# Performance work log

Hardware: AMD Instinct MI355X
Metric: run time of the kernel (lower is better)

The kernel has to match this reference:

```python
import jax, jax.numpy as jnp
import numpy as np

N, E = 50000, 800000
D, H, C, ED = 128, 8, 16, 4  # embed_dim, heads, head_dim, edge_dim


def _add_self_loops(edge_index, ea, n):
    # PyG add_self_loops with fill_value='mean': self-loop edge_attr is the
    # mean of incoming edge attributes per destination node (0 if none).
    src, dst = edge_index[0], edge_index[1]
    deg = jax.ops.segment_sum(jnp.ones((src.shape[0],), ea.dtype), dst, num_segments=n)
    loop_ea = jax.ops.segment_sum(ea, dst, num_segments=n) / jnp.maximum(deg, 1.0)[:, None]
    ar = jnp.arange(n, dtype=src.dtype)
    return (jnp.concatenate([src, ar]), jnp.concatenate([dst, ar]),
            jnp.concatenate([ea, loop_ea], axis=0))


def _gatv2(x, src, dst, ea, Wl, bl, Wr, br, We, att, bias, concat):
    n = x.shape[0]
    xl = (x @ Wl + bl).reshape(n, H, C)   # lin_l -> messages (source)
    xr = (x @ Wr + br).reshape(n, H, C)   # lin_r -> target
    e = (ea @ We).reshape(-1, H, C)       # lin_edge (no bias in PyG)
    m = jax.nn.leaky_relu(xl[src] + xr[dst] + e, negative_slope=0.2)  # [Etot,H,C]
    alpha = jnp.einsum('ehc,hc->eh', m, att)
    amax = jax.ops.segment_max(alpha, dst, num_segments=n)   # every node has a self loop
    ex = jnp.exp(alpha - amax[dst])
    den = jax.ops.segment_sum(ex, dst, num_segments=n)
    a = ex / den[dst]                                        # segment softmax over dst
    out = jax.ops.segment_sum(xl[src] * a[:, :, None], dst, num_segments=n)  # [N,H,C]
    out = out.reshape(n, H * C) if concat else out.mean(axis=1)
    return out + bias


def _ln(h, g, b):
    mu = h.mean(-1, keepdims=True)
    var = jnp.var(h, axis=-1, keepdims=True)
    return (h - mu) / jnp.sqrt(var + 1e-5) * g + b


def setup_inputs() -> dict:
    key = jax.random.key(0)
    ks = jax.random.split(key, 32)
    s = 0.05
    inp = {
        'x': jax.random.normal(ks[0], (N, D), jnp.float32),
        'edge_index': jax.random.randint(ks[1], (2, E), 0, N, jnp.int32),
        'edge_attr': jax.random.normal(ks[2], (E, ED), jnp.float32),
    }
    dims = [(D, H * C), (H * C, H * C), (H * C, C)]  # (in_dim, bias_dim per layer)
    k = 3
    for i, (din, bdim) in enumerate(dims):
        inp[f'Wl{i}'] = jax.random.normal(ks[k], (din, H * C), jnp.float32) * s; k += 1
        inp[f'bl{i}'] = jnp.zeros((H * C,), jnp.float32)
        inp[f'Wr{i}'] = jax.random.normal(ks[k], (din, H * C), jnp.float32) * s; k += 1
        inp[f'br{i}'] = jnp.zeros((H * C,), jnp.float32)
        inp[f'We{i}'] = jax.random.normal(ks[k], (ED, H * C), jnp.float32) * s; k += 1
        inp[f'att{i}'] = jax.random.normal(ks[k], (H, C), jnp.float32) * s; k += 1
        inp[f'b{i}'] = jnp.zeros((bdim,), jnp.float32)
        inp[f'g{i}'] = jnp.ones((bdim,), jnp.float32)
        inp[f'be{i}'] = jnp.zeros((bdim,), jnp.float32)
    inp['Wout'] = jax.random.normal(ks[k], (C, D), jnp.float32) * s
    inp['bout'] = jnp.zeros((D,), jnp.float32)
    return inp


def reference(x, edge_index, edge_attr,
              Wl0, bl0, Wr0, br0, We0, att0, b0, g0, be0,
              Wl1, bl1, Wr1, br1, We1, att1, b1, g1, be1,
              Wl2, bl2, Wr2, br2, We2, att2, b2, g2, be2,
              Wout, bout):
    n = x.shape[0]
    src, dst, ea = _add_self_loops(edge_index, edge_attr, n)
    layers = [
        (Wl0, bl0, Wr0, br0, We0, att0, b0, g0, be0, True),
        (Wl1, bl1, Wr1, br1, We1, att1, b1, g1, be1, True),
        (Wl2, bl2, Wr2, br2, We2, att2, b2, g2, be2, False),
    ]
    for (Wl, bl, Wr, br, We, att, bias, g, be, concat) in layers:
        h = _gatv2(x, src, dst, ea, Wl, bl, Wr, br, We, att, bias, concat)
        h = jax.nn.elu(h)
        h = _ln(h, g, be)
        if h.shape == x.shape:  # residual (layers 0,1)
            h = h + x
        x = h
    return x @ Wout + bout
```

## Files before the change

kernel.cpp:

```cpp
#include <hip/hip_runtime.h>
#include <hip/hip_bf16.h>

#define ND 128
#define NH 8
#define NC 16

static inline size_t alignup(size_t x){ return (x + 255) & ~size_t(255); }

__device__ __forceinline__ ushort f2bf(float f){
    __hip_bfloat16 h = __float2bfloat16(f);
    return *reinterpret_cast<ushort*>(&h);
}

__device__ __forceinline__ float hred8(float x){
    int y;
    y = __builtin_amdgcn_mov_dpp(__float_as_int(x), 0xB1, 0xF, 0xF, true);
    x += __int_as_float(y);
    y = __builtin_amdgcn_mov_dpp(__float_as_int(x), 0x4E, 0xF, 0xF, true);
    x += __int_as_float(y);
    y = __builtin_amdgcn_mov_dpp(__float_as_int(x), 0x141, 0xF, 0xF, true);
    x += __int_as_float(y);
    return x;
}


__global__ void hist_kernel(const int* __restrict__ dsts, int* __restrict__ deg, int E)
{
    int e = blockIdx.x * blockDim.x + threadIdx.x;
    if (e >= E) return;
    atomicAdd(&deg[dsts[e]], 1);
}

__global__ __launch_bounds__(1024) void scan_kernel(const int* __restrict__ deg,
                                                    int* __restrict__ rowstart, int n)
{
    __shared__ int wsum[16];
    int tid = threadIdx.x;
    int lane = tid & 63, wid = tid >> 6;
    int carry = 0;
    for (int base = 0; base < n; base += 1024) {
        int idx = base + tid;
        int v = (idx < n) ? ((deg[idx] + 3) & ~3) : 0;
        int s = v;
        #pragma unroll
        for (int o = 1; o < 64; o <<= 1) {
            int t = __shfl_up(s, o);
            if (lane >= o) s += t;
        }
        if (lane == 63) wsum[wid] = s;
        __syncthreads();
        int off = 0;
        #pragma unroll
        for (int w = 0; w < 16; ++w) {
            int ws_ = wsum[w];
            if (w < wid) off += ws_;
        }
        int total = 0;
        #pragma unroll
        for (int w = 0; w < 16; ++w) total += wsum[w];
        if (idx < n) rowstart[idx] = carry + off + (s - v);
        carry += total;
        __syncthreads();
    }
    if (tid == 0) rowstart[n] = carry;
}

__global__ void scatter_kernel(const int* __restrict__ srcs, const int* __restrict__ dsts,
                               const float4* __restrict__ ea4,
                               const int* __restrict__ rowstart, int* __restrict__ cursor,
                               int* __restrict__ src_sorted, float4* __restrict__ ea_sorted, int E)
{
    int e = blockIdx.x * blockDim.x + threadIdx.x;
    if (e >= E) return;
    int d = dsts[e];
    int pos = rowstart[d] + atomicAdd(&cursor[d], 1);
    src_sorted[pos] = srcs[e];
    ea_sorted[pos] = ea4[e];
}

__global__ void padfill_kernel(const int* __restrict__ rowstart, const int* __restrict__ deg,
                               int* __restrict__ src_sorted, float4* __restrict__ ea_sorted, int n)
{
    int v = blockIdx.x * blockDim.x + threadIdx.x;
    if (v < n) {
        int d = deg[v];
        int p = rowstart[v] + d;
        int pe = rowstart[v] + ((d + 3) & ~3);
        for (; p < pe; ++p) {
            src_sorted[p] = 0;
            ea_sorted[p] = make_float4(0.f, 0.f, 0.f, 0.f);
        }
    } else if (v < n + 64) {
        int p = rowstart[n] + (v - n);
        src_sorted[p] = 0;
        ea_sorted[p] = make_float4(0.f, 0.f, 0.f, 0.f);
    }
}


__global__ __launch_bounds__(256) void gemm_xw2(const float* __restrict__ X,
                                                const float* __restrict__ Wl,
                                                const float* __restrict__ bl,
                                                const float* __restrict__ Wr,
                                                const float* __restrict__ br,
                                                ushort* __restrict__ XLB,
                                                float* __restrict__ XR, int nrows)
{
    __shared__ float xs[64][128];
    int tid = threadIdx.x;
    int row0 = blockIdx.x * 64;

    const float4* X4 = (const float4*)X;
    float4* xs4 = (float4*)xs;
    #pragma unroll
    for (int i = tid; i < 64*32; i += 256) {
        int r = i >> 5;
        float4 v = make_float4(0.f, 0.f, 0.f, 0.f);
        if (row0 + r < nrows) v = X4[(size_t)(row0 + r) * 32 + (i & 31)];
        xs4[i] = v;
    }
    __syncthreads();

    int cg = tid & 31;
    int rg = (tid >> 5) * 8;
    float accl[8][4], accr[8][4];
    float4 blv = ((const float4*)bl)[cg];
    float4 brv = ((const float4*)br)[cg];
    #pragma unroll
    for (int r = 0; r < 8; r++) {
        accl[r][0] = blv.x; accl[r][1] = blv.y; accl[r][2] = blv.z; accl[r][3] = blv.w;
        accr[r][0] = brv.x; accr[r][1] = brv.y; accr[r][2] = brv.z; accr[r][3] = brv.w;
    }

    #pragma unroll 2
    for (int k = 0; k < 128; k++) {
        float4 wl = ((const float4*)(Wl + (size_t)k * 128))[cg];
        float4 wr = ((const float4*)(Wr + (size_t)k * 128))[cg];
        #pragma unroll
        for (int r = 0; r < 8; r++) {
            float xv = xs[rg + r][k];
            accl[r][0] = fmaf(xv, wl.x, accl[r][0]);
            accl[r][1] = fmaf(xv, wl.y, accl[r][1]);
            accl[r][2] = fmaf(xv, wl.z, accl[r][2]);
            accl[r][3] = fmaf(xv, wl.w, accl[r][3]);
            accr[r][0] = fmaf(xv, wr.x, accr[r][0]);
            accr[r][1] = fmaf(xv, wr.y, accr[r][1]);
            accr[r][2] = fmaf(xv, wr.z, accr[r][2]);
            accr[r][3] = fmaf(xv, wr.w, accr[r][3]);
        }
    }

    #pragma unroll
    for (int r = 0; r < 8; r++) {
        int row = row0 + rg + r;
        if (row < nrows) {
            ushort4 ob;
            ob.x = f2bf(accl[r][0]); ob.y = f2bf(accl[r][1]);
            ob.z = f2bf(accl[r][2]); ob.w = f2bf(accl[r][3]);
            ((ushort4*)XLB)[(size_t)row * 32 + cg] = ob;
            float4 of = make_float4(accr[r][0], accr[r][1], accr[r][2], accr[r][3]);
            ((float4*)XR)[(size_t)row * 32 + cg] = of;
        }
    }
}


__device__ __forceinline__ void gat_wave(
    int dstv, int t,
    const uint* __restrict__ xl_u, const float* __restrict__ xr,
    const int* __restrict__ rowstart, const int* __restrict__ deg,
    const int* __restrict__ src_sorted, const float4* __restrict__ ea_sorted,
    const float* __restrict__ We, const float* __restrict__ att,
    float& r0_out, float& r1_out, float& l_out)
{
    float2 xrv = ((const float2*)(xr + (size_t)dstv * ND))[t];
    float2 we0 = ((const float2*)(We))[t];
    float2 we1 = ((const float2*)(We + ND))[t];
    float2 we2 = ((const float2*)(We + 2*ND))[t];
    float2 we3 = ((const float2*)(We + 3*ND))[t];
    float2 attv = ((const float2*)att)[t];

    int p0 = rowstart[dstv];
    int dv = deg[dstv];
    int pads = (dv + 3) & ~3;

    uint xsw = xl_u[((size_t)dstv << 6) + t];

    const uint* xlt = xl_u + t;
    const int* sp = src_sorted + p0;
    const float4* ep = ea_sorted + p0;

    float s0=0.f, s1=0.f, s2=0.f, s3=0.f, lsum=0.f, a0=0.f, a1=0.f;

    int4 sA = *(const int4*)sp;
    uint xA0 = xlt[(size_t)sA.x << 6];
    uint xA1 = xlt[(size_t)sA.y << 6];
    uint xA2 = xlt[(size_t)sA.z << 6];
    uint xA3 = xlt[(size_t)sA.w << 6];
    int4 sB = *(const int4*)(sp + 4);

    for (int p = 0; p < pads; p += 4) {
        uint xB0 = xlt[(size_t)sB.x << 6];
        uint xB1 = xlt[(size_t)sB.y << 6];
        uint xB2 = xlt[(size_t)sB.z << 6];
        uint xB3 = xlt[(size_t)sB.w << 6];
        int4 sC = *(const int4*)(sp + p + 8);
        float4 ea0 = ep[p];
        float4 ea1 = ep[p + 1];
        float4 ea2 = ep[p + 2];
        float4 ea3 = ep[p + 3];

        float b00 = fmaf(ea0.x, we0.x, fmaf(ea0.y, we1.x, fmaf(ea0.z, we2.x, fmaf(ea0.w, we3.x, xrv.x))));
        float b01 = fmaf(ea0.x, we0.y, fmaf(ea0.y, we1.y, fmaf(ea0.z, we2.y, fmaf(ea0.w, we3.y, xrv.y))));
        float b10 = fmaf(ea1.x, we0.x, fmaf(ea1.y, we1.x, fmaf(ea1.z, we2.x, fmaf(ea1.w, we3.x, xrv.x))));
        float b11 = fmaf(ea1.x, we0.y, fmaf(ea1.y, we1.y, fmaf(ea1.z, we2.y, fmaf(ea1.w, we3.y, xrv.y))));
        float b20 = fmaf(ea2.x, we0.x, fmaf(ea2.y, we1.x, fmaf(ea2.z, we2.x, fmaf(ea2.w, we3.x, xrv.x))));
        float b21 = fmaf(ea2.x, we0.y, fmaf(ea2.y, we1.y, fmaf(ea2.z, we2.y, fmaf(ea2.w, we3.y, xrv.y))));
        float b30 = fmaf(ea3.x, we0.x, fmaf(ea3.y, we1.x, fmaf(ea3.z, we2.x, fmaf(ea3.w, we3.x, xrv.x))));
        float b31 = fmaf(ea3.x, we0.y, fmaf(ea3.y, we1.y, fmaf(ea3.z, we2.y, fmaf(ea3.w, we3.y, xrv.y))));

        s0 += ea0.x + ea1.x + ea2.x + ea3.x;
        s1 += ea0.y + ea1.y + ea2.y + ea3.y;
        s2 += ea0.z + ea1.z + ea2.z + ea3.z;
        s3 += ea0.w + ea1.w + ea2.w + ea3.w;

        float x00 = __uint_as_float(xA0 << 16), x01 = __uint_as_float(xA0 & 0xffff0000u);
        float x10 = __uint_as_float(xA1 << 16), x11 = __uint_as_float(xA1 & 0xffff0000u);
        float x20 = __uint_as_float(xA2 << 16), x21 = __uint_as_float(xA2 & 0xffff0000u);
        float x30 = __uint_as_float(xA3 << 16), x31 = __uint_as_float(xA3 & 0xffff0000u);

        float z;
        z = x00 + b00; float l00 = fmaxf(z, 0.2f * z);
        z = x01 + b01; float l01 = fmaxf(z, 0.2f * z);
        z = x10 + b10; float l10 = fmaxf(z, 0.2f * z);
        z = x11 + b11; float l11 = fmaxf(z, 0.2f * z);
        z = x20 + b20; float l20 = fmaxf(z, 0.2f * z);
        z = x21 + b21; float l21 = fmaxf(z, 0.2f * z);
        z = x30 + b30; float l30 = fmaxf(z, 0.2f * z);
        z = x31 + b31; float l31 = fmaxf(z, 0.2f * z);

        float pt0 = fmaf(l01, attv.y, l00 * attv.x);
        float pt1 = fmaf(l11, attv.y, l10 * attv.x);
        float pt2 = fmaf(l21, attv.y, l20 * attv.x);
        float pt3 = fmaf(l31, attv.y, l30 * attv.x);

        int rem = pads - p;
        int live = dv - p;
        pt1 = (live > 1) ? pt1 : -1e30f;
        pt2 = (live > 2) ? pt2 : -1e30f;
        pt3 = (live > 3) ? pt3 : -1e30f;
        (void)rem;

        float al0 = hred8(pt0);
        float al1 = hred8(pt1);
        float al2 = hred8(pt2);
        float al3 = hred8(pt3);

        float pe0 = __expf(al0);
        float pe1 = __expf(al1);
        float pe2 = __expf(al2);
        float pe3 = __expf(al3);
        lsum += (pe0 + pe1) + (pe2 + pe3);
        a0 = fmaf(pe0, x00, a0); a0 = fmaf(pe1, x10, a0);
        a0 = fmaf(pe2, x20, a0); a0 = fmaf(pe3, x30, a0);
        a1 = fmaf(pe0, x01, a1); a1 = fmaf(pe1, x11, a1);
        a1 = fmaf(pe2, x21, a1); a1 = fmaf(pe3, x31, a1);

        xA0 = xB0; xA1 = xB1; xA2 = xB2; xA3 = xB3;
        sB = sC;
    }

    float inv = 1.0f / (float)(dv > 0 ? dv : 1);
    float x0 = __uint_as_float(xsw << 16);
    float x1 = __uint_as_float(xsw & 0xffff0000u);
    float e0 = (s0 * we0.x + s1 * we1.x + s2 * we2.x + s3 * we3.x) * inv;
    float e1 = (s0 * we0.y + s1 * we1.y + s2 * we2.y + s3 * we3.y) * inv;
    float m0 = x0 + xrv.x + e0; m0 = fmaxf(m0, 0.2f * m0);
    float m1 = x1 + xrv.y + e1; m1 = fmaxf(m1, 0.2f * m1);
    float al = hred8(fmaf(m1, attv.y, m0 * attv.x));
    float pe = __expf(al);
    l_out = lsum + pe;
    r0_out = fmaf(pe, x0, a0);
    r1_out = fmaf(pe, x1, a1);
}

__global__ __launch_bounds__(256) void attn_concat(
    const ushort* __restrict__ xlb, const float* __restrict__ xr,
    const float* __restrict__ xin,
    const int* __restrict__ rowstart, const int* __restrict__ deg,
    const int* __restrict__ src_sorted, const float4* __restrict__ ea_sorted,
    const float* __restrict__ We, const float* __restrict__ att,
    const float* __restrict__ bias, const float* __restrict__ g, const float* __restrict__ be,
    float* __restrict__ out, int n)
{
    int wid = threadIdx.x >> 6;
    int t = threadIdx.x & 63;
    int dstv = blockIdx.x * 4 + wid;
    if (dstv >= n) return;

    float r0, r1, l;
    gat_wave(dstv, t, (const uint*)xlb, xr, rowstart, deg, src_sorted, ea_sorted, We, att, r0, r1, l);

    float2 bv = ((const float2*)bias)[t];
    float linv = 1.0f / l;
    float h0 = r0 * linv + bv.x;
    float h1 = r1 * linv + bv.y;
    h0 = h0 > 0.f ? h0 : (__expf(h0) - 1.0f);
    h1 = h1 > 0.f ? h1 : (__expf(h1) - 1.0f);

    float ss = h0 + h1, qq = h0*h0 + h1*h1;
    #pragma unroll
    for (int o = 1; o < 64; o <<= 1) { ss += __shfl_xor(ss, o); qq += __shfl_xor(qq, o); }
    float mu = ss * (1.0f / ND);
    float var = qq * (1.0f / ND) - mu * mu;
    float rstd = rsqrtf(var + 1e-5f);

    float2 gv = ((const float2*)g)[t];
    float2 bev = ((const float2*)be)[t];
    float2 xiv = ((const float2*)(xin + (size_t)dstv * ND))[t];
    float2 o2;
    o2.x = (h0 - mu) * rstd * gv.x + bev.x + xiv.x;
    o2.y = (h1 - mu) * rstd * gv.y + bev.y + xiv.y;
    ((float2*)(out + (size_t)dstv * ND))[t] = o2;
}

__global__ __launch_bounds__(256) void attn_final(
    const ushort* __restrict__ xlb, const float* __restrict__ xr,
    const int* __restrict__ rowstart, const int* __restrict__ deg,
    const int* __restrict__ src_sorted, const float4* __restrict__ ea_sorted,
    const float* __restrict__ We, const float* __restrict__ att,
    const float* __restrict__ b2, const float* __restrict__ g2, const float* __restrict__ be2,
    const float* __restrict__ Wout, const float* __restrict__ bout,
    float* __restrict__ out, int n)
{
    __shared__ float h16s[4][16];
    int wid = threadIdx.x >> 6;
    int t = threadIdx.x & 63;
    int dstv = blockIdx.x * 4 + wid;
    if (dstv >= n) return;

    float r0, r1, l;
    gat_wave(dstv, t, (const uint*)xlb, xr, rowstart, deg, src_sorted, ea_sorted, We, att, r0, r1, l);
    float linv = 1.0f / l;
    r0 *= linv; r1 *= linv;

    float v0 = r0, v1 = r1;
    #pragma unroll
    for (int o = 8; o < 64; o <<= 1) { v0 += __shfl_xor(v0, o); v1 += __shfl_xor(v1, o); }
    int cc = t & 7;
    float2 b2v = ((const float2*)b2)[cc];
    v0 = v0 * (1.0f / NH) + b2v.x;
    v1 = v1 * (1.0f / NH) + b2v.y;
    v0 = v0 > 0.f ? v0 : (__expf(v0) - 1.0f);
    v1 = v1 > 0.f ? v1 : (__expf(v1) - 1.0f);

    float ss = v0 + v1, qq = v0*v0 + v1*v1;
    #pragma unroll
    for (int o = 1; o < 8; o <<= 1) { ss += __shfl_xor(ss, o); qq += __shfl_xor(qq, o); }
    float mu = ss * (1.0f / NC);
    float var = qq * (1.0f / NC) - mu * mu;
    float rstd = rsqrtf(var + 1e-5f);
    float2 g2v = ((const float2*)g2)[cc];
    float2 be2v = ((const float2*)be2)[cc];
    float t0 = (v0 - mu) * rstd * g2v.x + be2v.x;
    float t1 = (v1 - mu) * rstd * g2v.y + be2v.y;

    if (t < 8) { h16s[wid][2*t] = t0; h16s[wid][2*t + 1] = t1; }

    float2 ov = ((const float2*)bout)[t];
    #pragma unroll
    for (int k = 0; k < NC; k++) {
        float hk = h16s[wid][k];
        float2 wv = ((const float2*)Wout)[k * 64 + t];
        ov.x = fmaf(hk, wv.x, ov.x);
        ov.y = fmaf(hk, wv.y, ov.y);
    }
    ((float2*)(out + (size_t)dstv * ND))[t] = ov;
}


extern "C" void kernel_launch(void* const* d_in, const int* in_sizes, int n_in,
                              void* d_out, int out_size, void* d_ws, size_t ws_size,
                              hipStream_t stream)
{
    const float* x_in = (const float*)d_in[0];
    const int*   ei   = (const int*)d_in[1];
    const float* ea   = (const float*)d_in[2];
    const int N = in_sizes[0] / ND;
    const int E = in_sizes[1] / 2;
    const int* srcs = ei;
    const int* dsts = ei + E;
    const float4* ea4 = (const float4*)ea;

    const float *Wl[3], *bl[3], *Wr[3], *br[3], *We[3], *att[3], *bb[3], *gg[3], *be[3];
    for (int l = 0; l < 3; l++) {
        int b = 3 + 9 * l;
        Wl[l]  = (const float*)d_in[b + 0];
        bl[l]  = (const float*)d_in[b + 1];
        Wr[l]  = (const float*)d_in[b + 2];
        br[l]  = (const float*)d_in[b + 3];
        We[l]  = (const float*)d_in[b + 4];
        att[l] = (const float*)d_in[b + 5];
        bb[l]  = (const float*)d_in[b + 6];
        gg[l]  = (const float*)d_in[b + 7];
        be[l]  = (const float*)d_in[b + 8];
    }
    const float* Wout = (const float*)d_in[30];
    const float* bout = (const float*)d_in[31];

    const size_t EP = (size_t)E + 3 * (size_t)N + 80;

    char* ws = (char*)d_ws;
    size_t off = 0;
    int* deg        = (int*)(ws + off);      off = alignup(off + (size_t)N * 4);
    int* cursor     = (int*)(ws + off);      off = alignup(off + (size_t)N * 4);
    size_t zero_bytes = off;
    int* rowstart   = (int*)(ws + off);      off = alignup(off + (size_t)(N + 1) * 4);
    int* src_sorted = (int*)(ws + off);      off = alignup(off + EP * 4);
    float4* ea_sorted = (float4*)(ws + off); off = alignup(off + EP * 16);
    ushort* xlb     = (ushort*)(ws + off);   off = alignup(off + (size_t)N * ND * 2);
    float* xr       = (float*)(ws + off);    off = alignup(off + (size_t)N * ND * 4);
    float* xa       = (float*)(ws + off);    off = alignup(off + (size_t)N * ND * 4);
    float* xb       = (float*)d_out;

    hipMemsetAsync(d_ws, 0, zero_bytes, stream);

    int ethreads = 256;
    int eblocks = (E + ethreads - 1) / ethreads;
    hist_kernel<<<eblocks, ethreads, 0, stream>>>(dsts, deg, E);
    scan_kernel<<<1, 1024, 0, stream>>>(deg, rowstart, N);
    padfill_kernel<<<(N + 64 + 255) / 256, 256, 0, stream>>>(rowstart, deg, src_sorted, ea_sorted, N);
    scatter_kernel<<<eblocks, ethreads, 0, stream>>>(srcs, dsts, ea4, rowstart, cursor,
                                                     src_sorted, ea_sorted, E);

    int gblocks = (N + 63) / 64;
    int ablocks = (N + 3) / 4;

    gemm_xw2<<<gblocks, 256, 0, stream>>>(x_in, Wl[0], bl[0], Wr[0], br[0], xlb, xr, N);
    attn_concat<<<ablocks, 256, 0, stream>>>(xlb, xr, x_in, rowstart, deg, src_sorted, ea_sorted,
                                             We[0], att[0], bb[0], gg[0], be[0], xa, N);
    gemm_xw2<<<gblocks, 256, 0, stream>>>(xa, Wl[1], bl[1], Wr[1], br[1], xlb, xr, N);
    attn_concat<<<ablocks, 256, 0, stream>>>(xlb, xr, xa, rowstart, deg, src_sorted, ea_sorted,
                                             We[1], att[1], bb[1], gg[1], be[1], xb, N);
    gemm_xw2<<<gblocks, 256, 0, stream>>>(xb, Wl[2], bl[2], Wr[2], br[2], xlb, xr, N);
    attn_final<<<ablocks, 256, 0, stream>>>(xlb, xr, rowstart, deg, src_sorted, ea_sorted,
                                            We[2], att[2], bb[2], gg[2], be[2],
                                            Wout, bout, (float*)d_out, N);
}
```

Measured before the change: 514.1 us.

## Vectorize GAT edge loop with packed float2 math and deepen gather prefetch

Rewrites the per-edge attention loop using 2-wide vector types so the compiler can emit packed FP32 ops (v_pk_fma/v_pk_mul) for the edge projection, leaky-relu input and weighted accumulation. It also deepens the software pipeline from one to two quads of prefetched source-feature gathers. Row start and degree are made wave-uniform with readfirstlane, and addressing uses 32-bit indices. The deeper prefetch raises register pressure and reads source indices further past the segment, and fmaf chains become separate mul/add, which may change rounding slightly.

```diff
diff --git a/kernel.cpp b/kernel.cpp
--- a/kernel.cpp
+++ b/kernel.cpp
@@ -5,11 +5,28 @@
 #define NH 8
 #define NC 16
 
+typedef float v2f __attribute__((ext_vector_type(2)));
+
 static inline size_t alignup(size_t x){ return (x + 255) & ~size_t(255); }
 
 __device__ __forceinline__ ushort f2bf(float f){
     __hip_bfloat16 h = __float2bfloat16(f);
     return *reinterpret_cast<ushort*>(&h);
+}
+
+__device__ __forceinline__ v2f unpack_bf2(uint u){
+    v2f r;
+    r.x = __uint_as_float(u << 16);
+    r.y = __uint_as_float(u & 0xffff0000u);
+    return r;
+}
+
+__device__ __forceinline__ v2f lrelu2(v2f z){
+    v2f s = z * 0.2f;
+    v2f r;
+    r.x = fmaxf(z.x, s.x);
+    r.y = fmaxf(z.y, s.y);
+    return r;
 }
 
 __device__ __forceinline__ float hred8(float x){
@@ -171,85 +188,84 @@
     const int* __restrict__ rowstart, const int* __restrict__ deg,
     const int* __restrict__ src_sorted, const float4* __restrict__ ea_sorted,
     const float* __restrict__ We, const float* __restrict__ att,
-    float& r0_out, float& r1_out, float& l_out)
-{
-    float2 xrv = ((const float2*)(xr + (size_t)dstv * ND))[t];
-    float2 we0 = ((const float2*)(We))[t];
-    float2 we1 = ((const float2*)(We + ND))[t];
-    float2 we2 = ((const float2*)(We + 2*ND))[t];
-    float2 we3 = ((const float2*)(We + 3*ND))[t];
-    float2 attv = ((const float2*)att)[t];
-
-    int p0 = rowstart[dstv];
-    int dv = deg[dstv];
+    v2f& r_out, float& l_out)
+{
+    v2f xrv  = ((const v2f*)(xr + (size_t)dstv * ND))[t];
+    v2f we0  = ((const v2f*)(We))[t];
+    v2f we1  = ((const v2f*)(We + ND))[t];
+    v2f we2  = ((const v2f*)(We + 2*ND))[t];
+    v2f we3  = ((const v2f*)(We + 3*ND))[t];
+    v2f attv = ((const v2f*)att)[t];
+
+    int p0 = __builtin_amdgcn_readfirstlane(rowstart[dstv]);
+    int dv = __builtin_amdgcn_readfirstlane(deg[dstv]);
     int pads = (dv + 3) & ~3;
 
-    uint xsw = xl_u[((size_t)dstv << 6) + t];
-
-    const uint* xlt = xl_u + t;
+    uint xsw = xl_u[(((uint)dstv) << 6) + t];
+
     const int* sp = src_sorted + p0;
     const float4* ep = ea_sorted + p0;
 
-    float s0=0.f, s1=0.f, s2=0.f, s3=0.f, lsum=0.f, a0=0.f, a1=0.f;
-
-    int4 sA = *(const int4*)sp;
-    uint xA0 = xlt[(size_t)sA.x << 6];
-    uint xA1 = xlt[(size_t)sA.y << 6];
-    uint xA2 = xlt[(size_t)sA.z << 6];
-    uint xA3 = xlt[(size_t)sA.w << 6];
+    v2f s01 = {0.f, 0.f}, s23 = {0.f, 0.f};
+    v2f a = {0.f, 0.f};
+    float lsum = 0.f;
+
+    int4 sA = *(const int4*)(sp);
+    uint xA0 = xl_u[(((uint)sA.x) << 6) + t];
+    uint xA1 = xl_u[(((uint)sA.y) << 6) + t];
+    uint xA2 = xl_u[(((uint)sA.z) << 6) + t];
+    uint xA3 = xl_u[(((uint)sA.w) << 6) + t];
     int4 sB = *(const int4*)(sp + 4);
+    uint xB0 = xl_u[(((uint)sB.x) << 6) + t];
+    uint xB1 = xl_u[(((uint)sB.y) << 6) + t];
+    uint xB2 = xl_u[(((uint)sB.z) << 6) + t];
+    uint xB3 = xl_u[(((uint)sB.w) << 6) + t];
+    int4 sC = *(const int4*)(sp + 8);
 
     for (int p = 0; p < pads; p += 4) {
-        uint xB0 = xlt[(size_t)sB.x << 6];
-        uint xB1 = xlt[(size_t)sB.y << 6];
-        uint xB2 = xlt[(size_t)sB.z << 6];
-        uint xB3 = xlt[(size_t)sB.w << 6];
-        int4 sC = *(const int4*)(sp + p + 8);
+        uint xC0 = xl_u[(((uint)sC.x) << 6) + t];
+        uint xC1 = xl_u[(((uint)sC.y) << 6) + t];
+        uint xC2 = xl_u[(((uint)sC.z) << 6) + t];
+        uint xC3 = xl_u[(((uint)sC.w) << 6) + t];
+        int4 sD = *(const int4*)(sp + p + 12);
         float4 ea0 = ep[p];
         float4 ea1 = ep[p + 1];
         float4 ea2 = ep[p + 2];
         float4 ea3 = ep[p + 3];
 
-        float b00 = fmaf(ea0.x, we0.x, fmaf(ea0.y, we1.x, fmaf(ea0.z, we2.x, fmaf(ea0.w, we3.x, xrv.x))));
-        float b01 = fmaf(ea0.x, we0.y, fmaf(ea0.y, we1.y, fmaf(ea0.z, we2.y, fmaf(ea0.w, we3.y, xrv.y))));
-        float b10 = fmaf(ea1.x, we0.x, fmaf(ea1.y, we1.x, fmaf(ea1.z, we2.x, fmaf(ea1.w, we3.x, xrv.x))));
-        float b11 = fmaf(ea1.x, we0.y, fmaf(ea1.y, we1.y, fmaf(ea1.z, we2.y, fmaf(ea1.w, we3.y, xrv.y))));
-        float b20 = fmaf(ea2.x, we0.x, fmaf(ea2.y, we1.x, fmaf(ea2.z, we2.x, fmaf(ea2.w, we3.x, xrv.x))));
-        float b21 = fmaf(ea2.x, we0.y, fmaf(ea2.y, we1.y, fmaf(ea2.z, we2.y, fmaf(ea2.w, we3.y, xrv.y))));
-        float b30 = fmaf(ea3.x, we0.x, fmaf(ea3.y, we1.x, fmaf(ea3.z, we2.x, fmaf(ea3.w, we3.x, xrv.x))));
-        float b31 = fmaf(ea3.x, we0.y, fmaf(ea3.y, we1.y, fmaf(ea3.z, we2.y, fmaf(ea3.w, we3.y, xrv.y))));
-
-        s0 += ea0.x + ea1.x + ea2.x + ea3.x;
-        s1 += ea0.y + ea1.y + ea2.y + ea3.y;
-        s2 += ea0.z + ea1.z + ea2.z + ea3.z;
-        s3 += ea0.w + ea1.w + ea2.w + ea3.w;
-
-        float x00 = __uint_as_float(xA0 << 16), x01 = __uint_as_float(xA0 & 0xffff0000u);
-        float x10 = __uint_as_float(xA1 << 16), x11 = __uint_as_float(xA1 & 0xffff0000u);
-        float x20 = __uint_as_float(xA2 << 16), x21 = __uint_as_float(xA2 & 0xffff0000u);
-        float x30 = __uint_as_float(xA3 << 16), x31 = __uint_as_float(xA3 & 0xffff0000u);
-
-        float z;
-        z = x00 + b00; float l00 = fmaxf(z, 0.2f * z);
-        z = x01 + b01; float l01 = fmaxf(z, 0.2f * z);
-        z = x10 + b10; float l10 = fmaxf(z, 0.2f * z);
-        z = x11 + b11; float l11 = fmaxf(z, 0.2f * z);
-        z = x20 + b20; float l20 = fmaxf(z, 0.2f * z);
-        z = x21 + b21; float l21 = fmaxf(z, 0.2f * z);
-        z = x30 + b30; float l30 = fmaxf(z, 0.2f * z);
-        z = x31 + b31; float l31 = fmaxf(z, 0.2f * z);
-
-        float pt0 = fmaf(l01, attv.y, l00 * attv.x);
-        float pt1 = fmaf(l11, attv.y, l10 * attv.x);
-        float pt2 = fmaf(l21, attv.y, l20 * attv.x);
-        float pt3 = fmaf(l31, attv.y, l30 * attv.x);
-
-        int rem = pads - p;
+        v2f b0 = xrv + we0*ea0.x + we1*ea0.y + we2*ea0.z + we3*ea0.w;
+        v2f b1 = xrv + we0*ea1.x + we1*ea1.y + we2*ea1.z + we3*ea1.w;
+        v2f b2 = xrv + we0*ea2.x + we1*ea2.y + we2*ea2.z + we3*ea2.w;
+        v2f b3 = xrv + we0*ea3.x + we1*ea3.y + we2*ea3.z + we3*ea3.w;
+
+        s01 += (v2f){ea0.x, ea0.y}; s23 += (v2f){ea0.z, ea0.w};
+        s01 += (v2f){ea1.x, ea1.y}; s23 += (v2f){ea1.z, ea1.w};
+        s01 += (v2f){ea2.x, ea2.y}; s23 += (v2f){ea2.z, ea2.w};
+        s01 += (v2f){ea3.x, ea3.y}; s23 += (v2f){ea3.z, ea3.w};
+
+        v2f x0 = unpack_bf2(xA0);
+        v2f x1 = unpack_bf2(xA1);
+        v2f x2 = unpack_bf2(xA2);
+        v2f x3 = unpack_bf2(xA3);
+
+        v2f l0 = lrelu2(x0 + b0);
+        v2f l1 = lrelu2(x1 + b1);
+        v2f l2 = lrelu2(x2 + b2);
+        v2f l3 = lrelu2(x3 + b3);
+
+        v2f q0 = l0 * attv;
+        v2f q1 = l1 * attv;
+        v2f q2 = l2 * attv;
+        v2f q3 = l3 * attv;
+        float pt0 = q0.x + q0.y;
+        float pt1 = q1.x + q1.y;
+        float pt2 = q2.x + q2.y;
+        float pt3 = q3.x + q3.y;
+
         int live = dv - p;
         pt1 = (live > 1) ? pt1 : -1e30f;
         pt2 = (live > 2) ? pt2 : -1e30f;
         pt3 = (live > 3) ? pt3 : -1e30f;
-        (void)rem;
 
         float al0 = hred8(pt0);
         float al1 = hred8(pt1);
@@ -261,27 +277,26 @@
         float pe2 = __expf(al2);
         float pe3 = __expf(al3);
         lsum += (pe0 + pe1) + (pe2 + pe3);
-        a0 = fmaf(pe0, x00, a0); a0 = fmaf(pe1, x10, a0);
-        a0 = fmaf(pe2, x20, a0); a0 = fmaf(pe3, x30, a0);
-        a1 = fmaf(pe0, x01, a1); a1 = fmaf(pe1, x11, a1);
-        a1 = fmaf(pe2, x21, a1); a1 = fmaf(pe3, x31, a1);
+        a += x0 * pe0;
+        a += x1 * pe1;
+        a += x2 * pe2;
+        a += x3 * pe3;
 
         xA0 = xB0; xA1 = xB1; xA2 = xB2; xA3 = xB3;
-        sB = sC;
+        xB0 = xC0; xB1 = xC1; xB2 = xC2; xB3 = xC3;
+        sC = sD;
     }
 
     float inv = 1.0f / (float)(dv > 0 ? dv : 1);
-    float x0 = __uint_as_float(xsw << 16);
-    float x1 = __uint_as_float(xsw & 0xffff0000u);
-    float e0 = (s0 * we0.x + s1 * we1.x + s2 * we2.x + s3 * we3.x) * inv;
-    float e1 = (s0 * we0.y + s1 * we1.y + s2 * we2.y + s3 * we3.y) * inv;
-    float m0 = x0 + xrv.x + e0; m0 = fmaxf(m0, 0.2f * m0);
-    float m1 = x1 + xrv.y + e1; m1 = fmaxf(m1, 0.2f * m1);
-    float al = hred8(fmaf(m1, attv.y, m0 * attv.x));
+    s01 *= inv; s23 *= inv;
+    v2f xs = unpack_bf2(xsw);
+    v2f bs = xrv + we0*s01.x + we1*s01.y + we2*s23.x + we3*s23.y;
+    v2f ls = lrelu2(xs + bs);
+    v2f qs = ls * attv;
+    float al = hred8(qs.x + qs.y);
     float pe = __expf(al);
     l_out = lsum + pe;
-    r0_out = fmaf(pe, x0, a0);
-    r1_out = fmaf(pe, x1, a1);
+    r_out = a + xs * pe;
 }
 
 __global__ __launch_bounds__(256) void attn_concat(
@@ -298,30 +313,27 @@
     int dstv = blockIdx.x * 4 + wid;
     if (dstv >= n) return;
 
-    float r0, r1, l;
-    gat_wave(dstv, t, (const uint*)xlb, xr, rowstart, deg, src_sorted, ea_sorted, We, att, r0, r1, l);
-
-    float2 bv = ((const float2*)bias)[t];
+    v2f av; float l;
+    gat_wave(dstv, t, (const uint*)xlb, xr, rowstart, deg, src_sorted, ea_sorted, We, att, av, l);
+
+    v2f bv = ((const v2f*)bias)[t];
     float linv = 1.0f / l;
-    float h0 = r0 * linv + bv.x;
-    float h1 = r1 * linv + bv.y;
-    h0 = h0 > 0.f ? h0 : (__expf(h0) - 1.0f);
-    h1 = h1 > 0.f ? h1 : (__expf(h1) - 1.0f);
-
-    float ss = h0 + h1, qq = h0*h0 + h1*h1;
+    v2f h = av * linv + bv;
+    h.x = h.x > 0.f ? h.x : (__expf(h.x) - 1.0f);
+    h.y = h.y > 0.f ? h.y : (__expf(h.y) - 1.0f);
+
+    float ss = h.x + h.y, qq = h.x*h.x + h.y*h.y;
     #pragma unroll
     for (int o = 1; o < 64; o <<= 1) { ss += __shfl_xor(ss, o); qq += __shfl_xor(qq, o); }
     float mu = ss * (1.0f / ND);
     float var = qq * (1.0f / ND) - mu * mu;
     float rstd = rsqrtf(var + 1e-5f);
 
-    float2 gv = ((const float2*)g)[t];
-    float2 bev = ((const float2*)be)[t];
-    float2 xiv = ((const float2*)(xin + (size_t)dstv * ND))[t];
-    float2 o2;
-    o2.x = (h0 - mu) * rstd * gv.x + bev.x + xiv.x;
-    o2.y = (h1 - mu) * rstd * gv.y + bev.y + xiv.y;
-    ((float2*)(out + (size_t)dstv * ND))[t] = o2;
+    v2f gv  = ((const v2f*)g)[t];
+    v2f bev = ((const v2f*)be)[t];
+    v2f xiv = ((const v2f*)(xin + (size_t)dstv * ND))[t];
+    v2f o2 = (h - mu) * rstd * gv + bev + xiv;
+    ((v2f*)(out + (size_t)dstv * ND))[t] = o2;
 }
 
 __global__ __launch_bounds__(256) void attn_final(
@@ -339,12 +351,11 @@
     int dstv = blockIdx.x * 4 + wid;
     if (dstv >= n) return;
 
-    float r0, r1, l;
-    gat_wave(dstv, t, (const uint*)xlb, xr, rowstart, deg, src_sorted, ea_sorted, We, att, r0, r1, l);
+    v2f av; float l;
+    gat_wave(dstv, t, (const uint*)xlb, xr, rowstart, deg, src_sorted, ea_sorted, We, att, av, l);
     float linv = 1.0f / l;
-    r0 *= linv; r1 *= linv;
-
-    float v0 = r0, v1 = r1;
+    float v0 = av.x * linv, v1 = av.y * linv;
+
     #pragma unroll
     for (int o = 8; o < 64; o <<= 1) { v0 += __shfl_xor(v0, o); v1 += __shfl_xor(v1, o); }
     int cc = t & 7;
```

Result: faster. 474.9 us (-7.6%).
